# Kernel tuning notes

Measured on AMD Instinct MI355X. Metric: run time of the kernel, lower is better.

Reference implementation:

```python
import jax, jax.numpy as jnp
from jax import lax
import numpy as np

# static config (matches init_kwargs)
B, H, Wd, C = 32, 96, 96, 64
nW, K, PAD = 4, 3, 1
WS = 48  # window_size = H // sqrt(nW)


def setup_inputs() -> dict:
    key = jax.random.key(0)
    ks = jax.random.split(key, 24)
    def p(i, shape, s=0.02):
        return jax.random.normal(ks[i], shape, dtype=jnp.float32) * s
    return {
        "x": jax.random.normal(ks[0], (B, H * Wd, C), dtype=jnp.float32),
        # se: conv1x1 -> gelu -> conv1x1 -> sigmoid
        "se_w1": p(1, (C, C)), "se_b1": p(2, (C,)),
        "se_w2": p(3, (C, C)), "se_b2": p(4, (C,)),
        # WinKernel_Reweight
        "dc_w": p(5, (nW, C)), "dc_b": p(6, (nW,)),            # grouped 1x1, nW groups of C->1
        "l1_w": p(7, (4 * nW, nW)), "l1_b": p(8, (4 * nW,)),
        "l2_w": p(9, (nW, 4 * nW)), "l2_b": p(10, (nW,)),
        # gk_fusion: grouped 1x1 (dim groups, nW->1 per group)
        "gkf_w": p(11, (C, nW)), "gkf_b": p(12, (C,)),
        # Fusion (gk_sum)
        "fu_proj_w": p(13, (C, nW, nW)), "fu_proj_b": p(14, (C * nW,)),  # grouped 1x1, dim groups of nW->nW
        "fu_fc1_w": p(15, (C, nW * C)), "fu_fc1_b": p(16, (C,)),
        "fu_fc2_w": p(17, (nW * C, C)), "fu_fc2_b": p(18, (nW * C,)),
        "fu_po_w": p(19, (C, C)), "fu_po_b": p(20, (C,)),
        # final proj_out
        "po_w": p(21, (C, C)), "po_b": p(22, (C,)),
    }


def _gelu(t):
    return jax.nn.gelu(t, approximate=False)  # torch nn.GELU default = exact erf


def _conv1x1(w, b, t):
    return jnp.einsum('oi,bihw->bohw', w, t) + b[None, :, None, None]


def _forward(x, se_w1, se_b1, se_w2, se_b2, dc_w, dc_b, l1_w, l1_b, l2_w, l2_b,
             gkf_w, gkf_b, fu_proj_w, fu_proj_b, fu_fc1_w, fu_fc1_b,
             fu_fc2_w, fu_fc2_b, fu_po_w, fu_po_b, po_w, po_b):
    xh = x.reshape(B, H, Wd, C)
    # window_partition -> (B*nW, C, WS, WS), windows row-major within each batch element
    win = (xh.reshape(B, 2, WS, 2, WS, C)
             .transpose(0, 1, 3, 2, 4, 5)
             .reshape(B * nW, WS, WS, C)
             .transpose(0, 3, 1, 2))
    # adaptive avg pool (WS->K, exact since WS % K == 0)
    pool = WS // K
    kern = win.reshape(B * nW, C, K, pool, K, pool).mean(axis=(3, 5))  # (B*nW, C, K, K)
    # SE block replaces kernels
    kern_se = jax.nn.sigmoid(_conv1x1(se_w2, se_b2, _gelu(_conv1x1(se_w1, se_b1, kern))))
    # WinKernel_Reweight
    xwin = win.reshape(B, nW * C, WS, WS)
    ww = xwin.mean(axis=(2, 3)).reshape(B, nW, C)                 # GAP then grouped 1x1 (nW groups)
    ww = jnp.einsum('wc,bwc->bw', dc_w, ww) + dc_b                # (B, nW)
    ww = _gelu(ww @ l1_w.T + l1_b)
    ww = jax.nn.sigmoid(ww @ l2_w.T + l2_b)                       # (B, nW)
    kr = kern_se.reshape(B, nW, C, K, K) * ww[:, :, None, None, None]
    # gk_fusion: after transpose(1,2) channel order is c-major; grouped conv -> per-c mix over windows
    gkf = jnp.einsum('cw,bwcij->bcij', gkf_w, kr) + gkf_b[None, :, None, None]  # (B, C, K, K)
    # Fusion (gk_sum) on SE kernels (window-major channel layout)
    feats_in = kern_se.reshape(B, nW * C, K, K)
    fg = feats_in.reshape(B, C, nW, K, K)                         # groups = consecutive nW channels
    feats = _gelu(jnp.einsum('goi,bgikl->bgokl', fu_proj_w, fg)
                  + fu_proj_b.reshape(1, C, nW, 1, 1))
    v = feats.mean(axis=(3, 4)).reshape(B, C * nW)                # GAP
    v = _gelu(v @ fu_fc1_w.T + fu_fc1_b)                          # (B, C)
    av = jax.nn.softmax((v @ fu_fc2_w.T + fu_fc2_b).reshape(B, nW, C), axis=1)
    x_sum = jnp.einsum('bwckl,bwc->bckl', feats_in.reshape(B, nW, C, K, K), av)
    gks = gkf + _conv1x1(fu_po_w, fu_po_b, x_sum)                 # (B, C, K, K)
    # assemble per-(sample, kernel-branch, channel) depthwise kernels and convolve
    gk = jnp.stack([gkf, gks], axis=1).reshape(B * 2 * C, 1, K, K)
    xi = jnp.broadcast_to(xh.transpose(0, 3, 1, 2)[:, None], (B, 2, C, H, Wd))
    xi = xi.reshape(1, B * 2 * C, H, Wd)
    y = lax.conv_general_dilated(xi, gk, window_strides=(1, 1),
                                 padding=((PAD, PAD), (PAD, PAD)),
                                 feature_group_count=B * 2 * C,
                                 dimension_numbers=('NCHW', 'OIHW', 'NCHW'))
    y = y.reshape(B, 2, C, H, Wd).sum(axis=1)                     # sum the two kernel branches
    y = _conv1x1(po_w, po_b, y)
    return y.transpose(0, 2, 3, 1).reshape(B, H * Wd, C)


def reference(x, se_w1, se_b1, se_w2, se_b2, dc_w, dc_b, l1_w, l1_b, l2_w, l2_b,
              gkf_w, gkf_b, fu_proj_w, fu_proj_b, fu_fc1_w, fu_fc1_b,
              fu_fc2_w, fu_fc2_b, fu_po_w, fu_po_b, po_w, po_b):
    return _forward(x, se_w1, se_b1, se_w2, se_b2, dc_w, dc_b, l1_w, l1_b, l2_w, l2_b,
                    gkf_w, gkf_b, fu_proj_w, fu_proj_b, fu_fc1_w, fu_fc1_b,
                    fu_fc2_w, fu_fc2_b, fu_po_w, fu_po_b, po_w, po_b)
```

## Files before the change

kernel.cpp:

```cpp
#include <hip/hip_runtime.h>
#include <hip/hip_bf16.h>

#define NPIX 9216

typedef __attribute__((ext_vector_type(8))) short short8v;
typedef __attribute__((ext_vector_type(4))) float floatx4;

__device__ __forceinline__ float geluf(float x){
  return 0.5f * x * (1.0f + erff(x * 0.70710678118654752440f));
}
__device__ __forceinline__ float sigm(float x){
  return 1.0f / (1.0f + expf(-x));
}
__device__ __forceinline__ unsigned short f2bf(float f){
  __hip_bfloat16 h = __float2bfloat16(f);
  return *(unsigned short*)&h;
}

__global__ __launch_bounds__(256) void k_pool(const float* __restrict__ x,
                                              const float* __restrict__ po_w,
                                              float* __restrict__ kern,
                                              unsigned short* __restrict__ frag_pw)
{
  int blk = blockIdx.x;
  int t = threadIdx.x;
  if (blk == 0){
    for (int idx=t; idx<4096; idx+=256){
      int f = idx >> 9, L = (idx >> 3) & 63, j = idx & 7;
      int nb = f >> 1, kb = f & 1;
      int o = nb*16 + (L & 15);
      int c = kb*32 + ((L >> 4) & 3)*8 + j;
      frag_pw[idx] = f2bf(po_w[o*64 + c]);
    }
  }
  int bw = blk / 9, rem = blk % 9;
  int ki = rem / 3, kj = rem % 3;
  int b = bw >> 2, w = bw & 3;
  int wr = w >> 1, wc = w & 1;
  int cg = t & 15, rw = t >> 4;
  int h = wr*48 + ki*16 + rw;
  int col0 = wc*48 + kj*16;
  size_t base = ((size_t)(b*NPIX + h*96 + col0))*64 + cg*4;
  float a0=0.f,a1=0.f,a2=0.f,a3=0.f;
  #pragma unroll
  for (int j=0;j<16;j++){
    float4 u = *(const float4*)(x + base + (size_t)j*64);
    a0 += u.x; a1 += u.y; a2 += u.z; a3 += u.w;
  }
  __shared__ float red[16*64];
  float* rr = &red[rw*64 + cg*4];
  rr[0]=a0; rr[1]=a1; rr[2]=a2; rr[3]=a3;
  __syncthreads();
  if (t < 64){
    float s = 0.f;
    #pragma unroll
    for (int r=0;r<16;r++) s += red[r*64 + t];
    kern[(size_t)bw*576 + t*9 + rem] = s * (1.0f/256.0f);
  }
}

__global__ __launch_bounds__(512) void k_fuse(const float* __restrict__ kern_ws,
    const float* __restrict__ se_w1, const float* __restrict__ se_b1,
    const float* __restrict__ se_w2, const float* __restrict__ se_b2,
    const float* __restrict__ dc_w,  const float* __restrict__ dc_b,
    const float* __restrict__ l1_w,  const float* __restrict__ l1_b,
    const float* __restrict__ l2_w,  const float* __restrict__ l2_b,
    const float* __restrict__ gkf_w, const float* __restrict__ gkf_b,
    const float* __restrict__ fu_proj_w, const float* __restrict__ fu_proj_b,
    const float* __restrict__ fu_fc1_w,  const float* __restrict__ fu_fc1_b,
    const float* __restrict__ fu_fc2_w,  const float* __restrict__ fu_fc2_b,
    const float* __restrict__ fu_po_w,   const float* __restrict__ fu_po_b,
    float* __restrict__ kc_ws)
{
  int b = blockIdx.x;
  int t = threadIdx.x;
  int lane = t & 63, wv = t >> 6;

  __shared__ float s_w1[64*65];
  __shared__ float s_w2[64*65];
  __shared__ float s_pow[64*65];
  __shared__ float s_kern[4*64*13];
  __shared__ float s_t1[4*64*13];
  __shared__ float s_kse[2304];
  __shared__ float s_prj[1088];
  __shared__ float s_feats[2304];
  __shared__ float s_gkf[576];
  __shared__ float s_xsum[576];
  __shared__ float s_wwc[256];
  __shared__ float s_v0[256];
  __shared__ float s_av[256];
  __shared__ float s_v1[64];
  __shared__ float s_small[64];

  for (int idx=t; idx<2304; idx+=512){
    int w = idx/576, cp = idx - w*576;
    int c = cp/9, p = cp - c*9;
    s_kern[(w*64+c)*13+p] = kern_ws[(size_t)(b*4+w)*576 + cp];
  }
  for (int j=t; j<4096; j+=512){
    int o=j>>6, i=j&63;
    s_w1[i*65+o]  = se_w1[j];
    s_w2[i*65+o]  = se_w2[j];
    s_pow[i*65+o] = fu_po_w[j];
  }
  for (int j=t; j<1024; j+=512){ int g=j>>4, oi=j&15; s_prj[g*17+oi] = fu_proj_w[j]; }
  __syncthreads();

  for (int idx=t; idx<2304; idx+=512){
    int o = idx & 63, wp = idx >> 6;
    int w = wp/9, p = wp - w*9;
    float acc = se_b1[o];
    #pragma unroll 8
    for (int i=0;i<64;i++) acc += s_w1[i*65+o]*s_kern[(w*64+i)*13+p];
    s_t1[(w*64+o)*13+p] = geluf(acc);
  }
  if (t < 256){
    const float* kr = &s_kern[t*13];
    float s = kr[0]+kr[1]+kr[2]+kr[3]+kr[4]+kr[5]+kr[6]+kr[7]+kr[8];
    s_wwc[t] = s * (1.0f/9.0f);
  }
  __syncthreads();

  for (int idx=t; idx<2304; idx+=512){
    int o = idx & 63, wp = idx >> 6;
    int w = wp/9, p = wp - w*9;
    float acc = se_b2[o];
    #pragma unroll 8
    for (int i=0;i<64;i++) acc += s_w2[i*65+o]*s_t1[(w*64+i)*13+p];
    s_kse[w*576 + o*9 + p] = sigm(acc);
  }
  if (t < 4){
    float acc = dc_b[t];
    #pragma unroll 8
    for (int c=0;c<64;c++) acc += dc_w[t*64+c]*s_wwc[t*64+c];
    s_small[t] = acc;
  }
  __syncthreads();

  for (int idx=t; idx<2304; idx+=512){
    int g = idx & 63, op = idx >> 6;
    int o = op/9, p = op - o*9;
    float acc = fu_proj_b[g*4+o];
    #pragma unroll
    for (int i=0;i<4;i++){
      int ch = g*4+i;
      acc += s_prj[g*17 + o*4 + i] * s_kse[(ch>>6)*576 + (ch&63)*9 + p];
    }
    s_feats[(g*4+o)*9 + p] = geluf(acc);
  }
  if (t < 16){
    float acc = l1_b[t];
    #pragma unroll
    for (int w=0;w<4;w++) acc += l1_w[t*4+w]*s_small[w];
    s_small[16+t] = geluf(acc);
  }
  __syncthreads();

  if (t < 256){
    const float* f = &s_feats[t*9];
    s_v0[t] = (f[0]+f[1]+f[2]+f[3]+f[4]+f[5]+f[6]+f[7]+f[8]) * (1.0f/9.0f);
  } else if (t < 260){
    int tt = t - 256;
    float acc = l2_b[tt];
    #pragma unroll
    for (int j=0;j<16;j++) acc += l2_w[tt*16+j]*s_small[16+j];
    s_small[32+tt] = sigm(acc);
  }
  __syncthreads();

  #pragma unroll
  for (int oi=0; oi<8; oi++){
    int o = wv*8 + oi;
    float v = fu_fc1_w[o*256 +       lane] * s_v0[      lane]
            + fu_fc1_w[o*256 +  64 + lane] * s_v0[ 64 + lane]
            + fu_fc1_w[o*256 + 128 + lane] * s_v0[128 + lane]
            + fu_fc1_w[o*256 + 192 + lane] * s_v0[192 + lane];
    #pragma unroll
    for (int m=32; m>0; m>>=1) v += __shfl_xor(v, m);
    if (lane == 0) s_v1[o] = geluf(v + fu_fc1_b[o]);
  }
  __syncthreads();

  if (t < 256){
    const float4* wr = (const float4*)(fu_fc2_w + t*64);
    float acc = 0.f;
    #pragma unroll
    for (int q=0;q<16;q++){
      float4 wq = wr[q];
      acc += wq.x*s_v1[q*4] + wq.y*s_v1[q*4+1] + wq.z*s_v1[q*4+2] + wq.w*s_v1[q*4+3];
    }
    s_av[t] = acc + fu_fc2_b[t];
  }
  for (int idx=t; idx<576; idx+=512){
    int c = idx & 63, p = idx >> 6;
    float acc = gkf_b[c];
    #pragma unroll
    for (int w=0;w<4;w++) acc += gkf_w[c*4+w]*s_kse[w*576+c*9+p]*s_small[32+w];
    s_gkf[c*9+p] = acc;
  }
  __syncthreads();

  if (t < 64){
    float z0=s_av[t], z1=s_av[64+t], z2=s_av[128+t], z3=s_av[192+t];
    float mx = fmaxf(fmaxf(z0,z1),fmaxf(z2,z3));
    float e0=expf(z0-mx), e1=expf(z1-mx), e2=expf(z2-mx), e3=expf(z3-mx);
    float inv = 1.0f/(e0+e1+e2+e3);
    s_av[t]=e0*inv; s_av[64+t]=e1*inv; s_av[128+t]=e2*inv; s_av[192+t]=e3*inv;
  }
  __syncthreads();

  for (int idx=t; idx<576; idx+=512){
    int c = idx & 63, p = idx >> 6;
    float s=0.f;
    #pragma unroll
    for (int w=0;w<4;w++) s += s_kse[w*576+c*9+p]*s_av[w*64+c];
    s_xsum[c*9+p] = s;
  }
  __syncthreads();

  for (int idx=t; idx<576; idx+=512){
    int c = idx & 63, p = idx >> 6;
    float acc = 2.0f*s_gkf[c*9+p] + fu_po_b[c];
    #pragma unroll 8
    for (int i=0;i<64;i++) acc += s_pow[i*65+c]*s_xsum[i*9+p];
    kc_ws[(size_t)b*576 + c*9 + p] = acc;
  }
}

__global__ __launch_bounds__(256, 4) void k_conv(const float* __restrict__ x,
                                                 const float* __restrict__ kc_ws,
                                                 const unsigned short* __restrict__ frag_pw,
                                                 const float* __restrict__ po_b,
                                                 float* __restrict__ out)
{
  int bi = blockIdx.x;
  int b = bi / 144, tile = bi % 144;
  int th = tile / 12, tw = tile % 12;
  int h0 = th*8, w0 = tw*8;
  int t = threadIdx.x;

  __shared__ float s_x[100*64];
  __shared__ unsigned short s_tmp[64*72];
  __shared__ float s_kc[576];

  if (th > 0 && th < 11 && tw > 0 && tw < 11){
    const float* xb = x + (((size_t)(b*NPIX + (h0-1)*96 + (w0-1)))<<6);
    for (int idx=t; idx<1600; idx+=256){
      int pix = idx >> 4, c4 = idx & 15;
      int r = pix / 10, col = pix - r*10;
      *(float4*)&s_x[pix*64 + c4*4] =
        *(const float4*)(xb + (((size_t)(r*96 + col))<<6) + c4*4);
    }
  } else {
    for (int idx=t; idx<1600; idx+=256){
      int pix = idx >> 4, c4 = idx & 15;
      int r = pix / 10, col = pix % 10;
      int hh = h0 - 1 + r, ww = w0 - 1 + col;
      float4 v = make_float4(0.f,0.f,0.f,0.f);
      if (hh >= 0 && hh < 96 && ww >= 0 && ww < 96)
        v = *(const float4*)(x + (((size_t)b*NPIX + hh*96 + ww)<<6) + c4*4);
      *(float4*)&s_x[pix*64 + c4*4] = v;
    }
  }
  for (int idx=t; idx<576; idx+=256) s_kc[idx] = kc_ws[b*576 + idx];
  __syncthreads();

  {
    int c = t & 63, rg = t >> 6;
    int r0 = rg*2;
    float k0=s_kc[c*9+0],k1=s_kc[c*9+1],k2=s_kc[c*9+2],
          k3=s_kc[c*9+3],k4=s_kc[c*9+4],k5=s_kc[c*9+5],
          k6=s_kc[c*9+6],k7=s_kc[c*9+7],k8=s_kc[c*9+8];
    float row[4][10];
    #pragma unroll
    for (int rr=0; rr<4; rr++)
      #pragma unroll
      for (int cc=0; cc<10; cc++)
        row[rr][cc] = s_x[((r0+rr)*10 + cc)*64 + c];
    #pragma unroll
    for (int dr=0; dr<2; dr++){
      int pr = r0 + dr;
      #pragma unroll
      for (int pc=0; pc<8; pc++){
        float acc = k0*row[dr+0][pc] + k1*row[dr+0][pc+1] + k2*row[dr+0][pc+2]
                  + k3*row[dr+1][pc] + k4*row[dr+1][pc+1] + k5*row[dr+1][pc+2]
                  + k6*row[dr+2][pc] + k7*row[dr+2][pc+1] + k8*row[dr+2][pc+2];
        s_tmp[(pr*8 + pc)*72 + c] = f2bf(acc);
      }
    }
  }
  __syncthreads();

  {
    int wv = t >> 6, lane = t & 63;
    int m = wv*16 + (lane & 15);
    int quad = lane >> 4;
    floatx4 acc[4] = {{0.f,0.f,0.f,0.f},{0.f,0.f,0.f,0.f},
                      {0.f,0.f,0.f,0.f},{0.f,0.f,0.f,0.f}};
    #pragma unroll
    for (int kb=0; kb<2; kb++){
      short8v afrag = *(const short8v*)&s_tmp[m*72 + kb*32 + quad*8];
      #pragma unroll
      for (int nb=0; nb<4; nb++){
        short8v bfrag = *(const short8v*)(frag_pw + (nb*2+kb)*512 + lane*8);
        acc[nb] = __builtin_amdgcn_mfma_f32_16x16x32_bf16(afrag, bfrag, acc[nb], 0, 0, 0);
      }
    }
    #pragma unroll
    for (int nb=0; nb<4; nb++){
      int o = nb*16 + (lane & 15);
      float pb = po_b[o];
      #pragma unroll
      for (int r=0; r<4; r++){
        int px = wv*16 + quad*4 + r;
        int hh = h0 + (px >> 3), wwp = w0 + (px & 7);
        __builtin_nontemporal_store(acc[nb][r] + pb,
            out + (((size_t)b*NPIX + hh*96 + wwp)<<6) + o);
      }
    }
  }
}

extern "C" void kernel_launch(void* const* d_in, const int* in_sizes, int n_in,
                              void* d_out, int out_size, void* d_ws, size_t ws_size,
                              hipStream_t stream) {
  const float* x        = (const float*)d_in[0];
  const float* se_w1    = (const float*)d_in[1];
  const float* se_b1    = (const float*)d_in[2];
  const float* se_w2    = (const float*)d_in[3];
  const float* se_b2    = (const float*)d_in[4];
  const float* dc_w     = (const float*)d_in[5];
  const float* dc_b     = (const float*)d_in[6];
  const float* l1_w     = (const float*)d_in[7];
  const float* l1_b     = (const float*)d_in[8];
  const float* l2_w     = (const float*)d_in[9];
  const float* l2_b     = (const float*)d_in[10];
  const float* gkf_w    = (const float*)d_in[11];
  const float* gkf_b    = (const float*)d_in[12];
  const float* fu_proj_w= (const float*)d_in[13];
  const float* fu_proj_b= (const float*)d_in[14];
  const float* fu_fc1_w = (const float*)d_in[15];
  const float* fu_fc1_b = (const float*)d_in[16];
  const float* fu_fc2_w = (const float*)d_in[17];
  const float* fu_fc2_b = (const float*)d_in[18];
  const float* fu_po_w  = (const float*)d_in[19];
  const float* fu_po_b  = (const float*)d_in[20];
  const float* po_w     = (const float*)d_in[21];
  const float* po_b     = (const float*)d_in[22];

  float* kern_ws = (float*)d_ws;
  float* kc_ws   = kern_ws + 73728;
  unsigned short* frag_pw = (unsigned short*)(kc_ws + 18432);

  k_pool<<<1152, 256, 0, stream>>>(x, po_w, kern_ws, frag_pw);
  k_fuse<<<32, 512, 0, stream>>>(kern_ws,
                                 se_w1, se_b1, se_w2, se_b2,
                                 dc_w, dc_b, l1_w, l1_b, l2_w, l2_b,
                                 gkf_w, gkf_b, fu_proj_w, fu_proj_b,
                                 fu_fc1_w, fu_fc1_b, fu_fc2_w, fu_fc2_b,
                                 fu_po_w, fu_po_b, kc_ws);
  k_conv<<<4608, 256, 0, stream>>>(x, kc_ws, frag_pw, po_b, (float*)d_out);
}
```

Measured before the change: 230.2 us.

## Alias conv LDS buffers, stage output for vector stores, remap block order

The separate shared buffers for the input halo, the bf16 intermediate and a new output staging area are merged into one aliased buffer, with extra barriers between phases. This cuts LDS use so more blocks fit per CU, and the launch-bounds hint rises from 4 to 5. MFMA results are written to LDS first and then stored to global as 16-byte vector nontemporal stores, replacing scattered scalar stores. Block indices are also permuted so neighbouring hardware blocks map to different batch/tile ranges, at the cost of three added __syncthreads.

```diff
diff --git a/kernel.cpp b/kernel.cpp
--- a/kernel.cpp
+++ b/kernel.cpp
@@ -227,28 +227,30 @@
   }
 }
 
-__global__ __launch_bounds__(256, 4) void k_conv(const float* __restrict__ x,
+__global__ __launch_bounds__(256, 5) void k_conv(const float* __restrict__ x,
                                                  const float* __restrict__ kc_ws,
                                                  const unsigned short* __restrict__ frag_pw,
                                                  const float* __restrict__ po_b,
                                                  float* __restrict__ out)
 {
-  int bi = blockIdx.x;
+  int bi_hw = blockIdx.x;
+  int bi = (bi_hw & 7) * 576 + (bi_hw >> 3);
   int b = bi / 144, tile = bi % 144;
   int th = tile / 12, tw = tile % 12;
   int h0 = th*8, w0 = tw*8;
   int t = threadIdx.x;
 
-  __shared__ float s_x[100*64];
-  __shared__ unsigned short s_tmp[64*72];
+  __shared__ __align__(16) float s_buf[6400];
   __shared__ float s_kc[576];
+  unsigned short* s_tmp = (unsigned short*)s_buf;
+  float* s_out = s_buf;
 
   if (th > 0 && th < 11 && tw > 0 && tw < 11){
     const float* xb = x + (((size_t)(b*NPIX + (h0-1)*96 + (w0-1)))<<6);
     for (int idx=t; idx<1600; idx+=256){
       int pix = idx >> 4, c4 = idx & 15;
       int r = pix / 10, col = pix - r*10;
-      *(float4*)&s_x[pix*64 + c4*4] =
+      *(float4*)&s_buf[pix*64 + c4*4] =
         *(const float4*)(xb + (((size_t)(r*96 + col))<<6) + c4*4);
     }
   } else {
@@ -259,24 +261,29 @@
       float4 v = make_float4(0.f,0.f,0.f,0.f);
       if (hh >= 0 && hh < 96 && ww >= 0 && ww < 96)
         v = *(const float4*)(x + (((size_t)b*NPIX + hh*96 + ww)<<6) + c4*4);
-      *(float4*)&s_x[pix*64 + c4*4] = v;
+      *(float4*)&s_buf[pix*64 + c4*4] = v;
     }
   }
   for (int idx=t; idx<576; idx+=256) s_kc[idx] = kc_ws[b*576 + idx];
   __syncthreads();
 
+  int c = t & 63, rg = t >> 6;
+  int r0 = rg*2;
+  float k0,k1,k2,k3,k4,k5,k6,k7,k8;
+  float row[4][10];
   {
-    int c = t & 63, rg = t >> 6;
-    int r0 = rg*2;
-    float k0=s_kc[c*9+0],k1=s_kc[c*9+1],k2=s_kc[c*9+2],
-          k3=s_kc[c*9+3],k4=s_kc[c*9+4],k5=s_kc[c*9+5],
-          k6=s_kc[c*9+6],k7=s_kc[c*9+7],k8=s_kc[c*9+8];
-    float row[4][10];
+    k0=s_kc[c*9+0];k1=s_kc[c*9+1];k2=s_kc[c*9+2];
+    k3=s_kc[c*9+3];k4=s_kc[c*9+4];k5=s_kc[c*9+5];
+    k6=s_kc[c*9+6];k7=s_kc[c*9+7];k8=s_kc[c*9+8];
     #pragma unroll
     for (int rr=0; rr<4; rr++)
       #pragma unroll
       for (int cc=0; cc<10; cc++)
-        row[rr][cc] = s_x[((r0+rr)*10 + cc)*64 + c];
+        row[rr][cc] = s_buf[((r0+rr)*10 + cc)*64 + c];
+  }
+  __syncthreads();
+
+  {
     #pragma unroll
     for (int dr=0; dr<2; dr++){
       int pr = r0 + dr;
@@ -291,12 +298,12 @@
   }
   __syncthreads();
 
+  int wv = t >> 6, lane = t & 63;
+  int quad = lane >> 4;
+  floatx4 acc[4] = {{0.f,0.f,0.f,0.f},{0.f,0.f,0.f,0.f},
+                    {0.f,0.f,0.f,0.f},{0.f,0.f,0.f,0.f}};
   {
-    int wv = t >> 6, lane = t & 63;
     int m = wv*16 + (lane & 15);
-    int quad = lane >> 4;
-    floatx4 acc[4] = {{0.f,0.f,0.f,0.f},{0.f,0.f,0.f,0.f},
-                      {0.f,0.f,0.f,0.f},{0.f,0.f,0.f,0.f}};
     #pragma unroll
     for (int kb=0; kb<2; kb++){
       short8v afrag = *(const short8v*)&s_tmp[m*72 + kb*32 + quad*8];
@@ -306,6 +313,10 @@
         acc[nb] = __builtin_amdgcn_mfma_f32_16x16x32_bf16(afrag, bfrag, acc[nb], 0, 0, 0);
       }
     }
+  }
+  __syncthreads();
+
+  {
     #pragma unroll
     for (int nb=0; nb<4; nb++){
       int o = nb*16 + (lane & 15);
@@ -313,11 +324,18 @@
       #pragma unroll
       for (int r=0; r<4; r++){
         int px = wv*16 + quad*4 + r;
-        int hh = h0 + (px >> 3), wwp = w0 + (px & 7);
-        __builtin_nontemporal_store(acc[nb][r] + pb,
-            out + (((size_t)b*NPIX + hh*96 + wwp)<<6) + o);
+        s_out[px*68 + o] = acc[nb][r] + pb;
       }
     }
+  }
+  __syncthreads();
+
+  for (int idx=t; idx<1024; idx+=256){
+    int px = idx >> 4, c4 = idx & 15;
+    int hh = h0 + (px >> 3), wwp = w0 + (px & 7);
+    floatx4 v = *(const floatx4*)&s_out[px*68 + c4*4];
+    __builtin_nontemporal_store(v,
+        (floatx4*)(out + (((size_t)b*NPIX + hh*96 + wwp)<<6) + c4*4));
   }
 }
 
```

New measurement: 222.2 us. 1.04x faster.
